# Performance work log

Measured on AMD Instinct MI355X. Metric: run time of the kernel, lower is better.

## Reference

```python
import jax, jax.numpy as jnp
import numpy as np
from jax import lax

B, T, K = 256, 512, 128


def setup_inputs() -> dict:
    key = jax.random.key(0)
    k1, k2, k3, k4 = jax.random.split(key, 4)
    tag_weights = jax.random.normal(k1, (B, T, K), dtype=jnp.float32)
    transition_weights = jax.random.normal(k2, (K, K), dtype=jnp.float32)
    # gold tags; -1 marks an unannotated (unclamped) position, as in partial CRF
    gold = jax.random.randint(k3, (B, T), -1, K)
    lengths = jax.random.randint(k4, (B,), 1, T + 1)
    return {"tag_weights": tag_weights, "transition_weights": transition_weights,
            "gold": gold, "lengths": lengths}


def _log_partition(tag_weights, transition, lengths):
    # tag_weights: [B,T,K], transition: [K,K] (trans[i,j] = score i->j), lengths: [B]
    Tt = tag_weights.shape[1]
    alpha0 = tag_weights[:, 0]                      # [B,K]
    emits = jnp.moveaxis(tag_weights[:, 1:], 1, 0)  # [T-1,B,K]
    ts = jnp.arange(1, Tt)

    def step(alpha, xs):
        emit, t = xs
        # stable logsumexp over previous tag i: [B,K_prev,1] + [1,K_prev,K_cur]
        new = jax.nn.logsumexp(alpha[:, :, None] + transition[None], axis=1) + emit
        # freeze alpha for finished sequences (t >= length)
        alpha = jnp.where((t < lengths)[:, None], new, alpha)
        return alpha, None

    alphaT, _ = lax.scan(step, alpha0, (emits, ts))
    return jax.nn.logsumexp(alphaT, axis=-1)  # [B]


def _clamp(tag_weights, gold, lengths):
    Bt, Tt, Kt = tag_weights.shape
    ar = jnp.arange(Kt)
    valid = jnp.arange(Tt)[None, :] < lengths[:, None]            # [B,T]
    allow = (gold[:, :, None] == ar[None, None, :]) | (gold[:, :, None] < 0)  # [B,T,K]
    # within length: only gold tag (or all if gold<0) allowed; beyond length the
    # recurrence is frozen so those positions are left unmasked (unused).
    mask = jnp.where(allow | ~valid[:, :, None], 0.0, -jnp.inf)
    return tag_weights + mask


def reference(tag_weights, transition_weights, gold, lengths):
    clamped = _clamp(tag_weights, gold, lengths)
    loss = (_log_partition(tag_weights, transition_weights, lengths)
            - _log_partition(clamped, transition_weights, lengths))
    return loss.mean()  # reduction='mean'
```

## Files before the change

kernel.cpp:

```cpp
#include <hip/hip_runtime.h>
#include <hip/hip_bf16.h>

#define B_DIM 256
#define T_DIM 512
#define K_DIM 128

__global__ __launch_bounds__(512) void crf_pass_kernel(
    const float* __restrict__ tw,
    const float* __restrict__ trans,
    const int*   __restrict__ gold,
    const int*   __restrict__ lengths,
    float*       __restrict__ wsv)
{
    const int bid = blockIdx.x;
    const int b = bid & (B_DIM - 1);
    const bool clamp = bid >= B_DIM;
    const int tid = threadIdx.x;
    const int k = tid & (K_DIM - 1);
    const int jq = tid >> 7;

    __shared__ __align__(16) float pbuf[K_DIM];
    __shared__ float part[4][K_DIM];

    float Ereg[32];
#pragma unroll
    for (int i = 0; i < 32; ++i)
        Ereg[i] = __expf(trans[(jq * 32 + i) * K_DIM + k]);

    const int len = lengths[b];
    const float* twb = tw + (size_t)b * T_DIM * K_DIM;
    const int* goldb = gold + b * T_DIM;

    float m;
    {
        float e_k = twb[k];
        float e_0 = twb[0];
        int g = clamp ? goldb[0] : -1;
        m = e_0;
        float p = __expf(e_k - e_0);
        if (g >= 0 && g != k) p = 0.0f;
        if (jq == 0) pbuf[k] = p;
    }
    __syncthreads();

    float curE[4], cur0[4]; int curG[4];
#pragma unroll
    for (int i = 0; i < 4; ++i) {
        int t = 1 + i; if (t > T_DIM - 1) t = T_DIM - 1;
        curE[i] = (jq == 0) ? twb[t * K_DIM + k] : 0.0f;
        cur0[i] = (jq == 0) ? twb[t * K_DIM] : 0.0f;
        curG[i] = (jq == 0 && clamp) ? goldb[t] : -1;
    }

    for (int tbase = 1; tbase < len; tbase += 4) {
        float nxtE[4], nxt0[4]; int nxtG[4];
#pragma unroll
        for (int i = 0; i < 4; ++i) {
            int t = tbase + 4 + i; if (t > T_DIM - 1) t = T_DIM - 1;
            nxtE[i] = (jq == 0) ? twb[t * K_DIM + k] : 0.0f;
            nxt0[i] = (jq == 0) ? twb[t * K_DIM] : 0.0f;
            nxtG[i] = (jq == 0 && clamp) ? goldb[t] : -1;
        }

#pragma unroll
        for (int i = 0; i < 4; ++i) {
            const int t = tbase + i;
            const bool live = (t < len);
            if (live) {
                float a0 = 0.f, a1 = 0.f, a2 = 0.f, a3 = 0.f;
                const float4* pv = (const float4*)&pbuf[jq * 32];
#pragma unroll
                for (int q = 0; q < 8; ++q) {
                    float4 pj = pv[q];
                    a0 = fmaf(pj.x, Ereg[4 * q + 0], a0);
                    a1 = fmaf(pj.y, Ereg[4 * q + 1], a1);
                    a2 = fmaf(pj.z, Ereg[4 * q + 2], a2);
                    a3 = fmaf(pj.w, Ereg[4 * q + 3], a3);
                }
                part[jq][k] = (a0 + a1) + (a2 + a3);
            }
            __syncthreads();
            if (live && jq == 0) {
                float s_k = ((part[0][k] + part[1][k]) + (part[2][k] + part[3][k]));
                float s_0 = ((part[0][0] + part[1][0]) + (part[2][0] + part[3][0]));
                float e0 = cur0[i], ek = curE[i]; int g = curG[i];
                m += __logf(s_0) + e0;
                float p = s_k * __builtin_amdgcn_rcpf(s_0) * __expf(ek - e0);
                if (g >= 0 && g != k) p = 0.0f;
                pbuf[k] = p;
            }
            __syncthreads();
        }
#pragma unroll
        for (int i = 0; i < 4; ++i) { curE[i] = nxtE[i]; cur0[i] = nxt0[i]; curG[i] = nxtG[i]; }
    }

    if (tid < 64) {
        float v = pbuf[tid] + pbuf[tid + 64];
#pragma unroll
        for (int off = 32; off; off >>= 1) v += __shfl_xor(v, off);
        if (tid == 0) wsv[bid] = m + __logf(v);
    }
}

__global__ void crf_finalize(const float* __restrict__ wsv, float* __restrict__ out)
{
    const int tid = threadIdx.x;
    float d = wsv[tid] - wsv[B_DIM + tid];
#pragma unroll
    for (int off = 32; off; off >>= 1) d += __shfl_xor(d, off);
    __shared__ float red[4];
    if ((tid & 63) == 0) red[tid >> 6] = d;
    __syncthreads();
    if (tid == 0) out[0] = (red[0] + red[1] + red[2] + red[3]) * (1.0f / (float)B_DIM);
}

extern "C" void kernel_launch(void* const* d_in, const int* in_sizes, int n_in,
                              void* d_out, int out_size, void* d_ws, size_t ws_size,
                              hipStream_t stream)
{
    const float* tw      = (const float*)d_in[0];
    const float* trans   = (const float*)d_in[1];
    const int*   gold    = (const int*)d_in[2];
    const int*   lengths = (const int*)d_in[3];
    float* wsv = (float*)d_ws;
    float* out = (float*)d_out;

    crf_pass_kernel<<<2 * B_DIM, 512, 0, stream>>>(tw, trans, gold, lengths, wsv);
    crf_finalize<<<1, B_DIM, 0, stream>>>(wsv, out);
}
```

Before: 342.9 us.

## Use one 128-thread block per sequence with full transition matrix in registers

Each block now uses 128 threads, and each thread keeps the entire 128-column exp(transition) vector in registers. This removes the 4-way split over previous tags and its partial-sum reduction through shared memory. The forward vector is double-buffered, so each timestep needs one barrier instead of two. Normalisation switches from dividing by element 0 to dividing by the full sum, which every thread recomputes redundantly. The cost is 128 floats of register pressure per thread and 4x more FMAs per thread, in exchange for shorter sync chains and higher block occupancy.

```diff
diff --git a/kernel.cpp b/kernel.cpp
--- a/kernel.cpp
+++ b/kernel.cpp
@@ -5,7 +5,7 @@
 #define T_DIM 512
 #define K_DIM 128
 
-__global__ __launch_bounds__(512) void crf_pass_kernel(
+__global__ __launch_bounds__(128, 1) void crf_pass_kernel(
     const float* __restrict__ tw,
     const float* __restrict__ trans,
     const int*   __restrict__ gold,
@@ -15,92 +15,87 @@
     const int bid = blockIdx.x;
     const int b = bid & (B_DIM - 1);
     const bool clamp = bid >= B_DIM;
-    const int tid = threadIdx.x;
-    const int k = tid & (K_DIM - 1);
-    const int jq = tid >> 7;
+    const int k = threadIdx.x;
 
-    __shared__ __align__(16) float pbuf[K_DIM];
-    __shared__ float part[4][K_DIM];
+    __shared__ __align__(16) float qbuf[2][K_DIM];
+    __shared__ float red[2];
 
-    float Ereg[32];
+    float E[K_DIM];
 #pragma unroll
-    for (int i = 0; i < 32; ++i)
-        Ereg[i] = __expf(trans[(jq * 32 + i) * K_DIM + k]);
+    for (int j = 0; j < K_DIM; ++j)
+        E[j] = __expf(trans[j * K_DIM + k]);
 
     const int len = lengths[b];
     const float* twb = tw + (size_t)b * T_DIM * K_DIM;
-    const int* goldb = gold + b * T_DIM;
+    const int* gb = gold + b * T_DIM;
 
-    float m;
+    float m = 0.0f;
+    float lastq;
     {
-        float e_k = twb[k];
-        float e_0 = twb[0];
-        int g = clamp ? goldb[0] : -1;
-        m = e_0;
-        float p = __expf(e_k - e_0);
-        if (g >= 0 && g != k) p = 0.0f;
-        if (jq == 0) pbuf[k] = p;
+        float e0 = twb[k];
+        int g = clamp ? gb[0] : -1;
+        float q = __expf(e0);
+        if (g >= 0 && g != k) q = 0.0f;
+        qbuf[0][k] = q;
+        lastq = q;
     }
     __syncthreads();
 
-    float curE[4], cur0[4]; int curG[4];
+    float ec[4]; int gc[4];
 #pragma unroll
     for (int i = 0; i < 4; ++i) {
         int t = 1 + i; if (t > T_DIM - 1) t = T_DIM - 1;
-        curE[i] = (jq == 0) ? twb[t * K_DIM + k] : 0.0f;
-        cur0[i] = (jq == 0) ? twb[t * K_DIM] : 0.0f;
-        curG[i] = (jq == 0 && clamp) ? goldb[t] : -1;
+        ec[i] = twb[t * K_DIM + k];
+        gc[i] = clamp ? gb[t] : -1;
     }
 
-    for (int tbase = 1; tbase < len; tbase += 4) {
-        float nxtE[4], nxt0[4]; int nxtG[4];
+    for (int t0 = 1; t0 < len; t0 += 4) {
+        float en[4]; int gn[4];
 #pragma unroll
         for (int i = 0; i < 4; ++i) {
-            int t = tbase + 4 + i; if (t > T_DIM - 1) t = T_DIM - 1;
-            nxtE[i] = (jq == 0) ? twb[t * K_DIM + k] : 0.0f;
-            nxt0[i] = (jq == 0) ? twb[t * K_DIM] : 0.0f;
-            nxtG[i] = (jq == 0 && clamp) ? goldb[t] : -1;
+            int t = t0 + 4 + i; if (t > T_DIM - 1) t = T_DIM - 1;
+            en[i] = twb[t * K_DIM + k];
+            gn[i] = clamp ? gb[t] : -1;
         }
 
 #pragma unroll
         for (int i = 0; i < 4; ++i) {
-            const int t = tbase + i;
-            const bool live = (t < len);
-            if (live) {
+            const int t = t0 + i;
+            if (t < len) {
+                const float4* qv = (const float4*)qbuf[(t - 1) & 1];
+                float x = __expf(ec[i]);
                 float a0 = 0.f, a1 = 0.f, a2 = 0.f, a3 = 0.f;
-                const float4* pv = (const float4*)&pbuf[jq * 32];
+                float r0 = 0.f, r1 = 0.f, r2 = 0.f, r3 = 0.f;
 #pragma unroll
-                for (int q = 0; q < 8; ++q) {
-                    float4 pj = pv[q];
-                    a0 = fmaf(pj.x, Ereg[4 * q + 0], a0);
-                    a1 = fmaf(pj.y, Ereg[4 * q + 1], a1);
-                    a2 = fmaf(pj.z, Ereg[4 * q + 2], a2);
-                    a3 = fmaf(pj.w, Ereg[4 * q + 3], a3);
+                for (int q4 = 0; q4 < 32; ++q4) {
+                    float4 pj = qv[q4];
+                    a0 = fmaf(pj.x, E[4 * q4 + 0], a0);
+                    a1 = fmaf(pj.y, E[4 * q4 + 1], a1);
+                    a2 = fmaf(pj.z, E[4 * q4 + 2], a2);
+                    a3 = fmaf(pj.w, E[4 * q4 + 3], a3);
+                    r0 += pj.x; r1 += pj.y; r2 += pj.z; r3 += pj.w;
                 }
-                part[jq][k] = (a0 + a1) + (a2 + a3);
-            }
-            __syncthreads();
-            if (live && jq == 0) {
-                float s_k = ((part[0][k] + part[1][k]) + (part[2][k] + part[3][k]));
-                float s_0 = ((part[0][0] + part[1][0]) + (part[2][0] + part[3][0]));
-                float e0 = cur0[i], ek = curE[i]; int g = curG[i];
-                m += __logf(s_0) + e0;
-                float p = s_k * __builtin_amdgcn_rcpf(s_0) * __expf(ek - e0);
-                if (g >= 0 && g != k) p = 0.0f;
-                pbuf[k] = p;
+                float s = (a0 + a1) + (a2 + a3);
+                float R = (r0 + r1) + (r2 + r3);
+                float qn = s * x * __builtin_amdgcn_rcpf(R);
+                int g = gc[i];
+                if (g >= 0 && g != k) qn = 0.0f;
+                qbuf[t & 1][k] = qn;
+                lastq = qn;
+                m += __logf(R);
             }
             __syncthreads();
         }
 #pragma unroll
-        for (int i = 0; i < 4; ++i) { curE[i] = nxtE[i]; cur0[i] = nxt0[i]; curG[i] = nxtG[i]; }
+        for (int i = 0; i < 4; ++i) { ec[i] = en[i]; gc[i] = gn[i]; }
     }
 
-    if (tid < 64) {
-        float v = pbuf[tid] + pbuf[tid + 64];
+    float v = lastq;
 #pragma unroll
-        for (int off = 32; off; off >>= 1) v += __shfl_xor(v, off);
-        if (tid == 0) wsv[bid] = m + __logf(v);
-    }
+    for (int off = 32; off; off >>= 1) v += __shfl_xor(v, off);
+    if ((k & 63) == 0) red[k >> 6] = v;
+    __syncthreads();
+    if (k == 0) wsv[bid] = m + __logf(red[0] + red[1]);
 }
 
 __global__ void crf_finalize(const float* __restrict__ wsv, float* __restrict__ out)
@@ -126,6 +121,6 @@
     float* wsv = (float*)d_ws;
     float* out = (float*)d_out;
 
-    crf_pass_kernel<<<2 * B_DIM, 512, 0, stream>>>(tw, trans, gold, lengths, wsv);
+    crf_pass_kernel<<<2 * B_DIM, 128, 0, stream>>>(tw, trans, gold, lengths, wsv);
     crf_finalize<<<1, B_DIM, 0, stream>>>(wsv, out);
 }
```

Result: slower. 736.1 us (+114.7%).
